# Kernel tuning notes

Measured on AMD Instinct MI355X. Metric: run time of the kernel, lower is better.

Reference implementation:

```python
import jax, jax.numpy as jnp
import numpy as np

B, D_IN, D_PROJ, N_CLS = 4096, 4096, 1024, 32
N_CHILD = (32, 64)


def setup_inputs() -> dict:
    key = jax.random.key(0)
    ks = jax.random.split(key, 12)
    std = 2e-05
    inp = {
        "x": jax.random.normal(ks[0], (B, D_IN), dtype=jnp.float32),
        "y": jax.random.randint(ks[1], (B,), 0, N_CLS, dtype=jnp.int32),
        # parent projection: Linear(D_IN, D_PROJ)
        "Wp": jax.random.normal(ks[2], (D_IN, D_PROJ), dtype=jnp.float32) * std,
        "bp": jnp.zeros((D_PROJ,), jnp.float32),
        # subclass projection: Linear(D_IN, D_PROJ)
        "Ws": jax.random.normal(ks[3], (D_IN, D_PROJ), dtype=jnp.float32) * std,
        "bs": jnp.zeros((D_PROJ,), jnp.float32),
        # parent classifier: Linear(D_PROJ, N_CLS)
        "Wc": jax.random.normal(ks[4], (D_PROJ, N_CLS), dtype=jnp.float32) * std,
        "bc": jnp.zeros((N_CLS,), jnp.float32),
        # child expert banks: level i has N_CLS experts of Linear(D_PROJ, N_CHILD[i])
        "cw0": jax.random.normal(ks[5], (N_CLS, N_CHILD[0], D_PROJ), dtype=jnp.float32) * std,
        "cb0": jnp.zeros((N_CLS, N_CHILD[0]), jnp.float32),
        "cw1": jax.random.normal(ks[6], (N_CLS, N_CHILD[1], D_PROJ), dtype=jnp.float32) * std,
        "cb1": jnp.zeros((N_CLS, N_CHILD[1]), jnp.float32),
    }
    return inp


def reference(x, y, Wp, bp, Ws, bs, Wc, bc, cw0, cb0, cw1, cb1):
    # dropout p = 0.0 -> identity
    parent_proj_embed = x @ Wp + bp                 # [B, D_PROJ]
    parent_logits = parent_proj_embed @ Wc + bc     # [B, N_CLS]
    child_proj_embed = x @ Ws + bs                  # [B, D_PROJ]
    # per-sample expert routing: gather the expert for label y[b], then batched matvec
    child_logits0 = jnp.einsum("bd,bnd->bn", child_proj_embed, cw0[y]) + cb0[y]  # [B, 32]
    child_logits1 = jnp.einsum("bd,bnd->bn", child_proj_embed, cw1[y]) + cb1[y]  # [B, 64]
    return (parent_logits, child_logits0, child_logits1, parent_proj_embed, child_proj_embed)
```

## Files before the change

kernel.cpp:

```cpp
#include <hip/hip_runtime.h>
#include <hip/hip_bf16.h>
#include <stdint.h>


typedef __attribute__((ext_vector_type(4))) float  floatx4;
typedef __attribute__((ext_vector_type(8))) short  shortx8;
typedef __attribute__((ext_vector_type(4))) short  shortx4;
typedef __attribute__((ext_vector_type(8))) __bf16 bf16x8;

static __device__ __forceinline__ ushort f32_to_bf16_rne(float f) {
  uint32_t u = __builtin_bit_cast(uint32_t, f);
  u += 0x7FFFu + ((u >> 16) & 1u);
  return (ushort)(u >> 16);
}

static __device__ __forceinline__ void async_copy16(const void* g, void* lds) {
  __builtin_amdgcn_global_load_lds(
      (__attribute__((address_space(1))) void*)(uintptr_t)g,
      (__attribute__((address_space(3))) void*)(uintptr_t)lds,
      16, 0, 0);
}

__global__ __launch_bounds__(256) void k_prep(
    const float* __restrict__ x,   const int* __restrict__ y,
    const float* __restrict__ Wp,  const float* __restrict__ Ws,
    const float* __restrict__ Wc,
    const float* __restrict__ cw0, const float* __restrict__ cw1,
    ushort* __restrict__ xb,  ushort* __restrict__ Bt1,
    ushort* __restrict__ cwb, ushort* __restrict__ Wcb,
    int* __restrict__ perm, int* __restrict__ offs)
{
  __shared__ __align__(16) ushort tile[64 * 72];
  __shared__ int hist[32], hbase[32], hcur[32];
  const int b = blockIdx.x;
  const int t = threadIdx.x;

  if (b < 2048) {
    const size_t base = (size_t)b * 8192 + t * 8;
    #pragma unroll
    for (int it = 0; it < 4; ++it) {
      const size_t i = base + it * 2048;
      floatx4 a = *reinterpret_cast<const floatx4*>(x + i);
      floatx4 c = *reinterpret_cast<const floatx4*>(x + i + 4);
      shortx8 o;
      o[0] = (short)f32_to_bf16_rne(a[0]); o[1] = (short)f32_to_bf16_rne(a[1]);
      o[2] = (short)f32_to_bf16_rne(a[2]); o[3] = (short)f32_to_bf16_rne(a[3]);
      o[4] = (short)f32_to_bf16_rne(c[0]); o[5] = (short)f32_to_bf16_rne(c[1]);
      o[6] = (short)f32_to_bf16_rne(c[2]); o[7] = (short)f32_to_bf16_rne(c[3]);
      *reinterpret_cast<shortx8*>(xb + i) = o;
    }
  } else if (b < 4096) {
    const int vt = b - 2048;
    const int z = vt >> 10, rest = vt & 1023;
    const int nt = rest >> 6, kt = rest & 63;
    const float* W = z ? Ws : Wp;
    const int r = t >> 4, c = (t & 15) * 4;
    #pragma unroll
    for (int j = 0; j < 4; ++j) {
      const int kk = r + j * 16;
      floatx4 v = *reinterpret_cast<const floatx4*>(
          W + (size_t)(kt * 64 + kk) * 1024 + nt * 64 + c);
      tile[(c + 0) * 72 + kk] = f32_to_bf16_rne(v[0]);
      tile[(c + 1) * 72 + kk] = f32_to_bf16_rne(v[1]);
      tile[(c + 2) * 72 + kk] = f32_to_bf16_rne(v[2]);
      tile[(c + 3) * 72 + kk] = f32_to_bf16_rne(v[3]);
    }
    __syncthreads();
    const int nl = t >> 3, ch = t & 7;
    #pragma unroll
    for (int j = 0; j < 2; ++j) {
      const int n = nl + j * 32;
      shortx8 v = *reinterpret_cast<const shortx8*>(tile + n * 72 + ch * 8);
      *reinterpret_cast<shortx8*>(
          Bt1 + (size_t)(z * 1024 + nt * 64 + n) * 4096 + kt * 64 + ch * 8) = v;
    }
  } else if (b < 4624) {
    const int k = t * 4;
    #pragma unroll 1
    for (int j = 0; j < 8; ++j) {
      const int row = (b - 4096) * 8 + j;
      float v0 = 0.f, v1 = 0.f, v2 = 0.f, v3 = 0.f;
      ushort* dst;
      if (row < 4096) {
        const int c = row >> 7, n = row & 127;
        if (n < 32) {
          floatx4 f = *reinterpret_cast<const floatx4*>(cw0 + (size_t)(c * 32 + n) * 1024 + k);
          v0 = f[0]; v1 = f[1]; v2 = f[2]; v3 = f[3];
        } else if (n < 96) {
          floatx4 f = *reinterpret_cast<const floatx4*>(cw1 + (size_t)(c * 64 + (n - 32)) * 1024 + k);
          v0 = f[0]; v1 = f[1]; v2 = f[2]; v3 = f[3];
        }
        dst = cwb + (size_t)row * 1024 + k;
      } else {
        const int n = row - 4096;
        if (n < 32) {
          v0 = Wc[(k + 0) * 32 + n]; v1 = Wc[(k + 1) * 32 + n];
          v2 = Wc[(k + 2) * 32 + n]; v3 = Wc[(k + 3) * 32 + n];
        }
        dst = Wcb + (size_t)n * 1024 + k;
      }
      shortx4 o;
      o[0] = (short)f32_to_bf16_rne(v0); o[1] = (short)f32_to_bf16_rne(v1);
      o[2] = (short)f32_to_bf16_rne(v2); o[3] = (short)f32_to_bf16_rne(v3);
      *reinterpret_cast<shortx4*>(dst) = o;
    }
  } else {
    if (t < 32) { hist[t] = 0; hcur[t] = 0; }
    __syncthreads();
    int yv[16];
    #pragma unroll
    for (int i = 0; i < 16; ++i) { yv[i] = y[t * 16 + i]; atomicAdd(&hist[yv[i]], 1); }
    __syncthreads();
    if (t == 0) {
      int s = 0;
      for (int c = 0; c < 32; ++c) { hbase[c] = s; offs[c] = s; s += hist[c]; }
      offs[32] = s;
    }
    __syncthreads();
    #pragma unroll
    for (int i = 0; i < 16; ++i) {
      const int c = yv[i];
      const int p = atomicAdd(&hcur[c], 1);
      perm[hbase[c] + p] = t * 16 + i;
    }
  }
}

__global__ __launch_bounds__(256) void k_gemm1(
    const ushort* __restrict__ xb, const ushort* __restrict__ Bt1,
    const float* __restrict__ bp, const float* __restrict__ bs,
    float* __restrict__ outP, float* __restrict__ outS,
    ushort* __restrict__ Pb, ushort* __restrict__ Sb)
{
  __shared__ __align__(16) ushort lA[128 * 128];
  __shared__ __align__(16) ushort lB[128 * 128];
  floatx4 acc[4][4];
  const floatx4 z4 = {0.f, 0.f, 0.f, 0.f};
  #pragma unroll
  for (int i = 0; i < 4; ++i)
    #pragma unroll
    for (int j = 0; j < 4; ++j) acc[i][j] = z4;

  const int t    = threadIdx.x;
  const int w    = t >> 6;
  const int lane = t & 63;
  const int wr   = w >> 1;
  const int wc   = w & 1;
  const int r16  = lane & 15;
  const int quad = lane >> 4;
  const int sr4  = lane >> 4;
  const int sc16 = lane & 15;

  const ushort* Abase = xb  + (size_t)(blockIdx.x * 128) * 4096;
  const ushort* Bbase = Bt1 + (size_t)(blockIdx.y * 128) * 4096;

  for (int k0 = 0; k0 < 4096; k0 += 128) {
    #pragma unroll
    for (int c2 = 0; c2 < 8; ++c2) {
      const int r  = 32 * w + 4 * c2 + sr4;
      const int gc = sc16 ^ (r & 15);
      async_copy16(Abase + (size_t)r * 4096 + k0 + gc * 8, lA + (32 * w + 4 * c2) * 128);
      async_copy16(Bbase + (size_t)r * 4096 + k0 + gc * 8, lB + (32 * w + 4 * c2) * 128);
    }
    __syncthreads();
    #pragma unroll
    for (int ks = 0; ks < 4; ++ks) {
      bf16x8 af[4], bfv[4];
      const int pc = (((ks * 4) + quad) ^ r16) * 8;
      #pragma unroll
      for (int mi = 0; mi < 4; ++mi)
        af[mi] = *reinterpret_cast<const bf16x8*>(lA + (wr * 64 + mi * 16 + r16) * 128 + pc);
      #pragma unroll
      for (int ni = 0; ni < 4; ++ni)
        bfv[ni] = *reinterpret_cast<const bf16x8*>(lB + (wc * 64 + ni * 16 + r16) * 128 + pc);
      #pragma unroll
      for (int mi = 0; mi < 4; ++mi)
        #pragma unroll
        for (int ni = 0; ni < 4; ++ni)
          acc[mi][ni] = __builtin_amdgcn_mfma_f32_16x16x32_bf16(
              af[mi], bfv[ni], acc[mi][ni], 0, 0, 0);
    }
    __syncthreads();
  }

  const int sel = (blockIdx.y >= 8);
  const float* bias = sel ? bs : bp;
  float*  outF = sel ? outS : outP;
  ushort* outB = sel ? Sb : Pb;
  const int colbase = blockIdx.y * 128 - sel * 1024;
  #pragma unroll
  for (int mi = 0; mi < 4; ++mi) {
    #pragma unroll
    for (int ni = 0; ni < 4; ++ni) {
      const int n = colbase + wc * 64 + ni * 16 + r16;
      const float bv = bias[n];
      #pragma unroll
      for (int rg = 0; rg < 4; ++rg) {
        const int m = blockIdx.x * 128 + wr * 64 + mi * 16 + quad * 4 + rg;
        const float v = acc[mi][ni][rg] + bv;
        const size_t off = (size_t)m * 1024 + n;
        outF[off] = v;
        outB[off] = f32_to_bf16_rne(v);
      }
    }
  }
}

__global__ __launch_bounds__(256) void k_head(
    const ushort* __restrict__ Sb, const ushort* __restrict__ Pb,
    const ushort* __restrict__ cwb, const ushort* __restrict__ Wcb,
    const int* __restrict__ perm, const int* __restrict__ off,
    const float* __restrict__ cb0, const float* __restrict__ cb1,
    const float* __restrict__ bc,
    float* __restrict__ out0, float* __restrict__ out1,
    float* __restrict__ outParent)
{
  __shared__ __align__(16) ushort lA[128 * 128];
  __shared__ __align__(16) ushort lB[128 * 128];
  floatx4 acc[4][4];
  const floatx4 z4 = {0.f, 0.f, 0.f, 0.f};
  #pragma unroll
  for (int i = 0; i < 4; ++i)
    #pragma unroll
    for (int j = 0; j < 4; ++j) acc[i][j] = z4;

  const int t = threadIdx.x, w = t >> 6, lane = t & 63;
  const int wr = w >> 1, wc = w & 1, r16 = lane & 15, quad = lane >> 4;
  const int sr4 = lane >> 4, sc16 = lane & 15;

  const int isParent = (blockIdx.y == 32);
  const int c    = isParent ? 0 : blockIdx.y;
  const int off0 = isParent ? 0 : off[c];
  const int cnt  = isParent ? 4096 : (off[c + 1] - off0);
  const int m0   = blockIdx.x * 128;
  if (m0 >= cnt) return;

  const ushort* Arow[8];
  #pragma unroll
  for (int c2 = 0; c2 < 8; ++c2) {
    const int r = 32 * w + 4 * c2 + sr4;
    if (isParent) Arow[c2] = Pb + (size_t)(m0 + r) * 1024;
    else          Arow[c2] = Sb + (size_t)perm[off0 + min(m0 + r, cnt - 1)] * 1024;
  }
  const ushort* Bbase = isParent ? Wcb : (cwb + (size_t)c * 128 * 1024);

  for (int k0 = 0; k0 < 1024; k0 += 128) {
    #pragma unroll
    for (int c2 = 0; c2 < 8; ++c2) {
      const int r  = 32 * w + 4 * c2 + sr4;
      const int gc = sc16 ^ (r & 15);
      async_copy16(Arow[c2] + k0 + gc * 8,                 lA + (32 * w + 4 * c2) * 128);
      async_copy16(Bbase + (size_t)r * 1024 + k0 + gc * 8, lB + (32 * w + 4 * c2) * 128);
    }
    __syncthreads();
    #pragma unroll
    for (int ks = 0; ks < 4; ++ks) {
      bf16x8 af[4], bfv[4];
      const int pc = (((ks * 4) + quad) ^ r16) * 8;
      #pragma unroll
      for (int mi = 0; mi < 4; ++mi)
        af[mi] = *reinterpret_cast<const bf16x8*>(lA + (wr * 64 + mi * 16 + r16) * 128 + pc);
      #pragma unroll
      for (int ni = 0; ni < 4; ++ni)
        bfv[ni] = *reinterpret_cast<const bf16x8*>(lB + (wc * 64 + ni * 16 + r16) * 128 + pc);
      #pragma unroll
      for (int mi = 0; mi < 4; ++mi)
        #pragma unroll
        for (int ni = 0; ni < 4; ++ni)
          acc[mi][ni] = __builtin_amdgcn_mfma_f32_16x16x32_bf16(
              af[mi], bfv[ni], acc[mi][ni], 0, 0, 0);
    }
    __syncthreads();
  }

  if (isParent) {
    if (wc == 0) {
      #pragma unroll
      for (int mi = 0; mi < 4; ++mi)
        #pragma unroll
        for (int ni = 0; ni < 2; ++ni) {
          const int n = ni * 16 + r16;
          const float bv = bc[n];
          #pragma unroll
          for (int rg = 0; rg < 4; ++rg) {
            const int m = m0 + wr * 64 + mi * 16 + quad * 4 + rg;
            outParent[(size_t)m * 32 + n] = acc[mi][ni][rg] + bv;
          }
        }
    }
    return;
  }

  #pragma unroll
  for (int mi = 0; mi < 4; ++mi) {
    #pragma unroll
    for (int rg = 0; rg < 4; ++rg) {
      const int gm = m0 + wr * 64 + mi * 16 + quad * 4 + rg;
      if (gm >= cnt) continue;
      const int sample = perm[off0 + gm];
      #pragma unroll
      for (int ni = 0; ni < 4; ++ni) {
        const int n = wc * 64 + ni * 16 + r16;
        if (n < 32)
          out0[(size_t)sample * 32 + n] = acc[mi][ni][rg] + cb0[c * 32 + n];
        else if (n < 96)
          out1[(size_t)sample * 64 + (n - 32)] = acc[mi][ni][rg] + cb1[c * 64 + (n - 32)];
      }
    }
  }
}


extern "C" void kernel_launch(void* const* d_in, const int* in_sizes, int n_in,
                              void* d_out, int out_size, void* d_ws, size_t ws_size,
                              hipStream_t stream) {
  const float* x   = (const float*)d_in[0];
  const int*   y   = (const int*)  d_in[1];
  const float* Wp  = (const float*)d_in[2];
  const float* bp  = (const float*)d_in[3];
  const float* Ws  = (const float*)d_in[4];
  const float* bs  = (const float*)d_in[5];
  const float* Wc  = (const float*)d_in[6];
  const float* bc  = (const float*)d_in[7];
  const float* cw0 = (const float*)d_in[8];
  const float* cb0 = (const float*)d_in[9];
  const float* cw1 = (const float*)d_in[10];
  const float* cb1 = (const float*)d_in[11];

  float* out = (float*)d_out;
  float* parent_logits = out;
  float* child0        = out + 131072;
  float* child1        = out + 262144;
  float* P             = out + 524288;
  float* S             = out + 4718592;

  char* ws = (char*)d_ws;
  ushort* xb   = (ushort*)(ws);
  ushort* Bt1  = (ushort*)(ws + 33554432);
  ushort* Pb   = (ushort*)(ws + 50331648);
  ushort* Sb   = (ushort*)(ws + 58720256);
  ushort* cwb  = (ushort*)(ws + 67108864);
  ushort* Wcb  = (ushort*)(ws + 75497472);
  int*    perm = (int*)   (ws + 75759616);
  int*    offs = (int*)   (ws + 75776000);

  k_prep <<<4625, 256, 0, stream>>>(x, y, Wp, Ws, Wc, cw0, cw1,
                                    xb, Bt1, cwb, Wcb, perm, offs);
  k_gemm1<<<dim3(32, 16), 256, 0, stream>>>(xb, Bt1, bp, bs, P, S, Pb, Sb);
  k_head <<<dim3(32, 33), 256, 0, stream>>>(Sb, Pb, cwb, Wcb, perm, offs,
                                            cb0, cb1, bc,
                                            child0, child1, parent_logits);
}
```

Before: 305.7 us.

## Split-K the head GEMM four ways with atomic accumulation into zeroed outputs

The head kernel's K loop is split across a new grid z-dimension of 4, each slice covering 256 of the 1024 reduction elements. Results are combined with float atomicAdd, and the bias is added only by the first slice. The prep kernel gets extra blocks that zero the logits region first. This raises the head kernel's block count so that many small per-expert tiles can fill the GPU, at the cost of atomic traffic and nondeterministic summation order.

Result: slower. 483.8 us (+58.2%).

```diff
diff --git a/kernel.cpp b/kernel.cpp
--- a/kernel.cpp
+++ b/kernel.cpp
@@ -28,7 +28,8 @@
     const float* __restrict__ cw0, const float* __restrict__ cw1,
     ushort* __restrict__ xb,  ushort* __restrict__ Bt1,
     ushort* __restrict__ cwb, ushort* __restrict__ Wcb,
-    int* __restrict__ perm, int* __restrict__ offs)
+    int* __restrict__ perm, int* __restrict__ offs,
+    float* __restrict__ outHead)
 {
   __shared__ __align__(16) ushort tile[64 * 72];
   __shared__ int hist[32], hbase[32], hcur[32];
@@ -104,7 +105,7 @@
       o[2] = (short)f32_to_bf16_rne(v2); o[3] = (short)f32_to_bf16_rne(v3);
       *reinterpret_cast<shortx4*>(dst) = o;
     }
-  } else {
+  } else if (b == 4624) {
     if (t < 32) { hist[t] = 0; hcur[t] = 0; }
     __syncthreads();
     int yv[16];
@@ -123,6 +124,12 @@
       const int p = atomicAdd(&hcur[c], 1);
       perm[hbase[c] + p] = t * 16 + i;
     }
+  } else {
+    const floatx4 z4 = {0.f, 0.f, 0.f, 0.f};
+    const size_t base = (size_t)(b - 4625) * 4096 + t * 4;
+    #pragma unroll
+    for (int j = 0; j < 4; ++j)
+      *reinterpret_cast<floatx4*>(outHead + base + j * 1024) = z4;
   }
 }
 
@@ -228,6 +235,7 @@
   const int wr = w >> 1, wc = w & 1, r16 = lane & 15, quad = lane >> 4;
   const int sr4 = lane >> 4, sc16 = lane & 15;
 
+  const int kz       = blockIdx.z;
   const int isParent = (blockIdx.y == 32);
   const int c    = isParent ? 0 : blockIdx.y;
   const int off0 = isParent ? 0 : off[c];
@@ -244,7 +252,7 @@
   }
   const ushort* Bbase = isParent ? Wcb : (cwb + (size_t)c * 128 * 1024);
 
-  for (int k0 = 0; k0 < 1024; k0 += 128) {
+  for (int k0 = kz * 256; k0 < kz * 256 + 256; k0 += 128) {
     #pragma unroll
     for (int c2 = 0; c2 < 8; ++c2) {
       const int r  = 32 * w + 4 * c2 + sr4;
@@ -280,11 +288,11 @@
         #pragma unroll
         for (int ni = 0; ni < 2; ++ni) {
           const int n = ni * 16 + r16;
-          const float bv = bc[n];
+          const float bv = (kz == 0) ? bc[n] : 0.f;
           #pragma unroll
           for (int rg = 0; rg < 4; ++rg) {
             const int m = m0 + wr * 64 + mi * 16 + quad * 4 + rg;
-            outParent[(size_t)m * 32 + n] = acc[mi][ni][rg] + bv;
+            atomicAdd(&outParent[(size_t)m * 32 + n], acc[mi][ni][rg] + bv);
           }
         }
     }
@@ -301,10 +309,13 @@
       #pragma unroll
       for (int ni = 0; ni < 4; ++ni) {
         const int n = wc * 64 + ni * 16 + r16;
-        if (n < 32)
-          out0[(size_t)sample * 32 + n] = acc[mi][ni][rg] + cb0[c * 32 + n];
-        else if (n < 96)
-          out1[(size_t)sample * 64 + (n - 32)] = acc[mi][ni][rg] + cb1[c * 64 + (n - 32)];
+        if (n < 32) {
+          const float bv = (kz == 0) ? cb0[c * 32 + n] : 0.f;
+          atomicAdd(&out0[(size_t)sample * 32 + n], acc[mi][ni][rg] + bv);
+        } else if (n < 96) {
+          const float bv = (kz == 0) ? cb1[c * 64 + (n - 32)] : 0.f;
+          atomicAdd(&out1[(size_t)sample * 64 + (n - 32)], acc[mi][ni][rg] + bv);
+        }
       }
     }
   }
@@ -344,10 +355,10 @@
   int*    perm = (int*)   (ws + 75759616);
   int*    offs = (int*)   (ws + 75776000);
 
-  k_prep <<<4625, 256, 0, stream>>>(x, y, Wp, Ws, Wc, cw0, cw1,
-                                    xb, Bt1, cwb, Wcb, perm, offs);
+  k_prep <<<4753, 256, 0, stream>>>(x, y, Wp, Ws, Wc, cw0, cw1,
+                                    xb, Bt1, cwb, Wcb, perm, offs, out);
   k_gemm1<<<dim3(32, 16), 256, 0, stream>>>(xb, Bt1, bp, bs, P, S, Pb, Sb);
-  k_head <<<dim3(32, 33), 256, 0, stream>>>(Sb, Pb, cwb, Wcb, perm, offs,
-                                            cb0, cb1, bc,
-                                            child0, child1, parent_logits);
-}
+  k_head <<<dim3(32, 33, 4), 256, 0, stream>>>(Sb, Pb, cwb, Wcb, perm, offs,
+                                               cb0, cb1, bc,
+                                               child0, child1, parent_logits);
+}
```

## Split-K the routed head GEMM four ways and add a reduction kernel

Applied to the files above, without the earlier changes.

Splits the head kernel's K=1024 loop into four 256-wide slices across blockIdx.z and writes unbiased partial sums to workspace, reusing the xb region. A new reduce kernel sums the four partials per sample and adds the class-specific or parent bias. The aim is more blocks in the head GEMM, which otherwise has few active tiles because of per-class routing. The cost is an extra launch and extra global traffic for the partial buffers.

New measurement: 317.3 us. 1.04x slower.

```diff
diff --git a/kernel.cpp b/kernel.cpp
--- a/kernel.cpp
+++ b/kernel.cpp
@@ -210,10 +210,7 @@
     const ushort* __restrict__ Sb, const ushort* __restrict__ Pb,
     const ushort* __restrict__ cwb, const ushort* __restrict__ Wcb,
     const int* __restrict__ perm, const int* __restrict__ off,
-    const float* __restrict__ cb0, const float* __restrict__ cb1,
-    const float* __restrict__ bc,
-    float* __restrict__ out0, float* __restrict__ out1,
-    float* __restrict__ outParent)
+    float* __restrict__ pcChild, float* __restrict__ pcPar)
 {
   __shared__ __align__(16) ushort lA[128 * 128];
   __shared__ __align__(16) ushort lB[128 * 128];
@@ -228,6 +225,7 @@
   const int wr = w >> 1, wc = w & 1, r16 = lane & 15, quad = lane >> 4;
   const int sr4 = lane >> 4, sc16 = lane & 15;
 
+  const int kz       = blockIdx.z;
   const int isParent = (blockIdx.y == 32);
   const int c    = isParent ? 0 : blockIdx.y;
   const int off0 = isParent ? 0 : off[c];
@@ -244,7 +242,7 @@
   }
   const ushort* Bbase = isParent ? Wcb : (cwb + (size_t)c * 128 * 1024);
 
-  for (int k0 = 0; k0 < 1024; k0 += 128) {
+  for (int k0 = kz * 256; k0 < kz * 256 + 256; k0 += 128) {
     #pragma unroll
     for (int c2 = 0; c2 < 8; ++c2) {
       const int r  = 32 * w + 4 * c2 + sr4;
@@ -280,11 +278,10 @@
         #pragma unroll
         for (int ni = 0; ni < 2; ++ni) {
           const int n = ni * 16 + r16;
-          const float bv = bc[n];
           #pragma unroll
           for (int rg = 0; rg < 4; ++rg) {
             const int m = m0 + wr * 64 + mi * 16 + quad * 4 + rg;
-            outParent[(size_t)m * 32 + n] = acc[mi][ni][rg] + bv;
+            pcPar[((size_t)kz * 4096 + m) * 32 + n] = acc[mi][ni][rg];
           }
         }
     }
@@ -301,12 +298,44 @@
       #pragma unroll
       for (int ni = 0; ni < 4; ++ni) {
         const int n = wc * 64 + ni * 16 + r16;
-        if (n < 32)
-          out0[(size_t)sample * 32 + n] = acc[mi][ni][rg] + cb0[c * 32 + n];
-        else if (n < 96)
-          out1[(size_t)sample * 64 + (n - 32)] = acc[mi][ni][rg] + cb1[c * 64 + (n - 32)];
+        if (n < 96)
+          pcChild[((size_t)kz * 4096 + sample) * 96 + n] = acc[mi][ni][rg];
       }
     }
+  }
+}
+
+__global__ __launch_bounds__(256) void k_reduce(
+    const float* __restrict__ pcChild, const float* __restrict__ pcPar,
+    const int* __restrict__ y,
+    const float* __restrict__ cb0, const float* __restrict__ cb1,
+    const float* __restrict__ bc,
+    float* __restrict__ out0, float* __restrict__ out1,
+    float* __restrict__ outParent)
+{
+  const int b = blockIdx.x;
+  const int t = threadIdx.x;
+  if (b < 512) {
+    const int s = b * 8 + (t >> 5);
+    const int cls = y[s];
+    #pragma unroll
+    for (int j = 0; j < 3; ++j) {
+      const int n = (t & 31) + 32 * j;
+      float v = pcChild[((size_t)0 * 4096 + s) * 96 + n]
+              + pcChild[((size_t)1 * 4096 + s) * 96 + n]
+              + pcChild[((size_t)2 * 4096 + s) * 96 + n]
+              + pcChild[((size_t)3 * 4096 + s) * 96 + n];
+      if (n < 32) out0[(size_t)s * 32 + n]        = v + cb0[cls * 32 + n];
+      else        out1[(size_t)s * 64 + (n - 32)] = v + cb1[cls * 64 + (n - 32)];
+    }
+  } else {
+    const int s = (b - 512) * 8 + (t >> 5);
+    const int n = t & 31;
+    float v = pcPar[((size_t)0 * 4096 + s) * 32 + n]
+            + pcPar[((size_t)1 * 4096 + s) * 32 + n]
+            + pcPar[((size_t)2 * 4096 + s) * 32 + n]
+            + pcPar[((size_t)3 * 4096 + s) * 32 + n];
+    outParent[(size_t)s * 32 + n] = v + bc[n];
   }
 }
 
@@ -335,19 +364,22 @@
   float* S             = out + 4718592;
 
   char* ws = (char*)d_ws;
-  ushort* xb   = (ushort*)(ws);
-  ushort* Bt1  = (ushort*)(ws + 33554432);
-  ushort* Pb   = (ushort*)(ws + 50331648);
-  ushort* Sb   = (ushort*)(ws + 58720256);
-  ushort* cwb  = (ushort*)(ws + 67108864);
-  ushort* Wcb  = (ushort*)(ws + 75497472);
-  int*    perm = (int*)   (ws + 75759616);
-  int*    offs = (int*)   (ws + 75776000);
-
-  k_prep <<<4625, 256, 0, stream>>>(x, y, Wp, Ws, Wc, cw0, cw1,
-                                    xb, Bt1, cwb, Wcb, perm, offs);
-  k_gemm1<<<dim3(32, 16), 256, 0, stream>>>(xb, Bt1, bp, bs, P, S, Pb, Sb);
-  k_head <<<dim3(32, 33), 256, 0, stream>>>(Sb, Pb, cwb, Wcb, perm, offs,
-                                            cb0, cb1, bc,
-                                            child0, child1, parent_logits);
-}
+  ushort* xb      = (ushort*)(ws);
+  float*  pcChild = (float*)(ws);
+  float*  pcPar   = (float*)(ws + 6291456);
+  ushort* Bt1     = (ushort*)(ws + 33554432);
+  ushort* Pb      = (ushort*)(ws + 50331648);
+  ushort* Sb      = (ushort*)(ws + 58720256);
+  ushort* cwb     = (ushort*)(ws + 67108864);
+  ushort* Wcb     = (ushort*)(ws + 75497472);
+  int*    perm    = (int*)   (ws + 75759616);
+  int*    offs    = (int*)   (ws + 75776000);
+
+  k_prep  <<<4625, 256, 0, stream>>>(x, y, Wp, Ws, Wc, cw0, cw1,
+                                     xb, Bt1, cwb, Wcb, perm, offs);
+  k_gemm1 <<<dim3(32, 16), 256, 0, stream>>>(xb, Bt1, bp, bs, P, S, Pb, Sb);
+  k_head  <<<dim3(32, 33, 4), 256, 0, stream>>>(Sb, Pb, cwb, Wcb, perm, offs,
+                                                pcChild, pcPar);
+  k_reduce<<<640, 256, 0, stream>>>(pcChild, pcPar, y, cb0, cb1, bc,
+                                    child0, child1, parent_logits);
+}
```
